# Optimization experiments

Measured on AMD Instinct MI355X. Metric: run time of the kernel, lower is better.

The kernel has to match this reference:

```python
import jax, jax.numpy as jnp
import numpy as np

N = 8192
IN_F = 128
OUT_F = 64
NEG_SLOPE = 0.2


def setup_inputs() -> dict:
    key = jax.random.key(0)
    k1, k2, k3, k4 = jax.random.split(key, 4)
    x = jax.random.normal(k1, (N, IN_F), dtype=jnp.float32)
    adj = jax.random.randint(k2, (N, N), 0, 2, dtype=jnp.int32)
    W = jax.random.normal(k3, (IN_F, OUT_F), dtype=jnp.float32) * (1.414 / np.sqrt(IN_F))
    a = jax.random.normal(k4, (2 * OUT_F, 1), dtype=jnp.float32) * 0.5
    return {"x": x, "adj": adj, "W": W, "a": a}


def reference(x, adj, W, a):
    # Wh: [N, F]
    Wh = x @ W
    # Decomposed pairwise score: e_ij = leaky_relu(Wh_i . a1 + Wh_j . a2)
    # identical math to the original [N*N, 2F] concat @ a construction.
    a1 = a[:OUT_F, 0]   # [F]
    a2 = a[OUT_F:, 0]   # [F]
    s1 = Wh @ a1        # [N]
    s2 = Wh @ a2        # [N]
    e = jax.nn.leaky_relu(s1[:, None] + s2[None, :], negative_slope=NEG_SLOPE)  # [N, N]
    # NOTE: the original zeros out non-edges (NOT -inf) before softmax.
    att = jnp.where(adj > 0, e, jnp.zeros_like(e))
    att = jax.nn.softmax(att, axis=1)
    return att @ Wh  # [N, F]
```

## Files before the change

kernel.cpp:

```cpp
#include <hip/hip_runtime.h>
#include <hip/hip_bf16.h>

#define N_NODES 8192
#define IN_FEAT 128
#define OUT_FEAT 64
#define NEG_SLOPE 0.2f
#define TILES (N_NODES / 16)
#define SUBC 256
#define NSUB (N_NODES / SUBC)
#define KPW 2
#define ROWPAD 272
#define BUFSZ (16 * ROWPAD)
#define LOG2E 1.44269504088896340736f

using f32x4  = __attribute__((ext_vector_type(4))) float;
using i32x4  = __attribute__((ext_vector_type(4))) int;
using bf16x8 = __attribute__((ext_vector_type(8))) short;

static __device__ __forceinline__ short f2bf(float f) {
    unsigned int u = __float_as_uint(f);
    unsigned int r = (u + 0x7FFFu + ((u >> 16) & 1u)) >> 16;
    return (short)r;
}

static __device__ __forceinline__ short f2bf_fast(float f) {
    __hip_bfloat16 h = __float2bfloat16(f);
    return __builtin_bit_cast(short, h);
}

static __device__ __forceinline__ float exp2_fast(float x) {
    return __builtin_amdgcn_exp2f(x);
}

__global__ __launch_bounds__(256) void k_wh(
    const float* __restrict__ x, const float* __restrict__ W,
    const float* __restrict__ a,
    float* __restrict__ s1, float* __restrict__ s2,
    unsigned short* __restrict__ whb)
{
    __shared__ float xs[4][IN_FEAT];
    const int wv   = threadIdx.x >> 6;
    const int lane = threadIdx.x & 63;
    const int row  = blockIdx.x * 4 + wv;

    const float2 xv = *(const float2*)(x + (size_t)row * IN_FEAT + lane * 2);
    xs[wv][lane * 2]     = xv.x;
    xs[wv][lane * 2 + 1] = xv.y;
    __syncthreads();

    float acc = 0.f;
    #pragma unroll
    for (int k = 0; k < IN_FEAT; ++k)
        acc = fmaf(xs[wv][k], W[k * OUT_FEAT + lane], acc);

    float p1 = acc * a[lane];
    float p2 = acc * a[OUT_FEAT + lane];
    #pragma unroll
    for (int off = 32; off; off >>= 1) {
        p1 += __shfl_xor(p1, off);
        p2 += __shfl_xor(p2, off);
    }
    if (lane == 0) {
        s1[row] = p1 * LOG2E;
        s2[row] = p2 * LOG2E;
    }

    const int jb = row >> 5;
    const int ri = row & 31;
    const int gl = ri >> 3;
    const int e  = ri & 7;
    const int fg = lane >> 4;
    const int cl = lane & 15;
    whb[(((size_t)(jb * 4 + fg) * 64) + (gl * 16 + cl)) * 8 + e] = (unsigned short)f2bf(acc);
}

__global__ __launch_bounds__(512, 6) void k_fused(
    const int* __restrict__ adj, const float* __restrict__ s1v,
    const float* __restrict__ s2v, const unsigned short* __restrict__ whb,
    float* __restrict__ out)
{
    __shared__ __align__(16) char lds[2 * BUFSZ + N_NODES * 4 + 256];
    char*  bufs = lds;
    float* s2l  = (float*)(lds + 2 * BUFSZ);
    float* zl   = (float*)(lds + 2 * BUFSZ + N_NODES * 4);
    float* red  = s2l;

    const int tid  = threadIdx.x;
    const int lane = tid & 63;
    const int w    = tid >> 6;
    const int tile = blockIdx.x;
    const int cl = lane & 15, g = lane >> 4;

    {
        const float* src = s2v + tid * 4;
        #pragma unroll
        for (int i = 0; i < 4; ++i)
            *(f32x4*)(s2l + tid * 4 + i * 2048) = *(const f32x4*)(src + i * 2048);
    }

    if (w < 4) {
        const int* stg = adj + ((size_t)(tile * 16 + w * 4)) * N_NODES + lane * 4;
        i32x4 ldA[4], ldB[4];

        auto issue = [&](i32x4 (&ld)[4], int c) {
            #pragma unroll
            for (int rr = 0; rr < 4; ++rr)
                ld[rr] = *(const i32x4*)(stg + (size_t)rr * N_NODES + c * SUBC);
        };
        auto pack = [&](i32x4 (&ld)[4], int c) {
            char* wbuf = bufs + (c & 1) * BUFSZ;
            #pragma unroll
            for (int rr = 0; rr < 4; ++rr) {
                i32x4 v = ld[rr];
                unsigned int d = (v[0] > 0 ? 1u : 0u) | (v[1] > 0 ? 0x100u : 0u)
                               | (v[2] > 0 ? 0x10000u : 0u) | (v[3] > 0 ? 0x1000000u : 0u);
                *(unsigned int*)(wbuf + (w * 4 + rr) * ROWPAD + lane * 4) = d;
            }
        };

        issue(ldA, 0);
        issue(ldB, 1);
        pack(ldA, 0);
        asm volatile("s_waitcnt lgkmcnt(0)" ::: "memory");
        __builtin_amdgcn_s_barrier();

        for (int c = 0; c < NSUB; c += 2) {
            if (c + 2 < NSUB) issue(ldA, c + 2);
            __builtin_amdgcn_sched_barrier(0);
            pack(ldB, c + 1);
            __builtin_amdgcn_sched_barrier(0);
            asm volatile("s_waitcnt lgkmcnt(0)" ::: "memory");
            __builtin_amdgcn_s_barrier();
            if (c + 3 < NSUB) issue(ldB, c + 3);
            __builtin_amdgcn_sched_barrier(0);
            if (c + 2 < NSUB) pack(ldA, c + 2);
            __builtin_amdgcn_sched_barrier(0);
            asm volatile("s_waitcnt lgkmcnt(0)" ::: "memory");
            __builtin_amdgcn_s_barrier();
        }

        __builtin_amdgcn_s_barrier();
        f32x4 rs = {0.f, 0.f, 0.f, 0.f};
        #pragma unroll
        for (int w2 = 0; w2 < 4; ++w2)
            rs += *(const f32x4*)(red + ((size_t)(w2 * 64 + lane)) * 16 + 4 * w);
        #pragma unroll
        for (int q = 0; q < 4; ++q) {
            const int rit = g * 4 + q;
            const float z = zl[rit] + zl[16 + rit] + zl[32 + rit] + zl[48 + rit];
            out[(size_t)(tile * 16 + rit) * OUT_FEAT + w * 16 + cl] = rs[q] / z;
        }
    } else {
        const int cw  = w - 4;
        const int row = tile * 16 + cl;
        const float s1r = s1v[row];

        f32x4 acc0 = {0.f, 0.f, 0.f, 0.f};
        f32x4 acc1 = acc0, acc2 = acc0, acc3 = acc0;
        float zacc = 0.f;

        asm volatile("s_waitcnt lgkmcnt(0)" ::: "memory");
        __builtin_amdgcn_s_barrier();

        for (int c = 0; c < NSUB; ++c) {
            const char* rbuf = bufs + (c & 1) * BUFSZ;
            #pragma unroll
            for (int kk = 0; kk < KPW; ++kk) {
                const int ks = cw * KPW + kk;
                const uint2 ab = *(const uint2*)(rbuf + cl * ROWPAD + ks * 32 + 8 * g);
                const float* sp = s2l + c * SUBC + ks * 32 + 8 * g;
                const f32x4 s0  = *(const f32x4*)(sp);
                const f32x4 s1x = *(const f32x4*)(sp + 4);
                const unsigned short* wq = whb + ((size_t)(c * 8 + ks)) * 2048 + lane * 8;
                bf16x8 B0 = *(const bf16x8*)(wq);
                bf16x8 B1 = *(const bf16x8*)(wq + 512);
                bf16x8 B2 = *(const bf16x8*)(wq + 1024);
                bf16x8 B3 = *(const bf16x8*)(wq + 1536);

                bf16x8 af;
                #pragma unroll
                for (int e = 0; e < 4; ++e) {
                    float tv = s1r + s0[e];
                    float el = fmaxf(tv, NEG_SLOPE * tv);
                    float wv = ((ab.x >> (8 * e)) & 1u) ? exp2_fast(el) : 1.0f;
                    zacc += wv;
                    af[e] = f2bf_fast(wv);
                }
                #pragma unroll
                for (int e = 0; e < 4; ++e) {
                    float tv = s1r + s1x[e];
                    float el = fmaxf(tv, NEG_SLOPE * tv);
                    float wv = ((ab.y >> (8 * e)) & 1u) ? exp2_fast(el) : 1.0f;
                    zacc += wv;
                    af[4 + e] = f2bf_fast(wv);
                }

                acc0 = __builtin_amdgcn_mfma_f32_16x16x32_bf16(af, B0, acc0, 0, 0, 0);
                acc1 = __builtin_amdgcn_mfma_f32_16x16x32_bf16(af, B1, acc1, 0, 0, 0);
                acc2 = __builtin_amdgcn_mfma_f32_16x16x32_bf16(af, B2, acc2, 0, 0, 0);
                acc3 = __builtin_amdgcn_mfma_f32_16x16x32_bf16(af, B3, acc3, 0, 0, 0);
            }
            asm volatile("s_waitcnt lgkmcnt(0)" ::: "memory");
            __builtin_amdgcn_s_barrier();
        }

        *(f32x4*)(red + ((size_t)(cw * 64 + lane)) * 16 + 0)  = acc0;
        *(f32x4*)(red + ((size_t)(cw * 64 + lane)) * 16 + 4)  = acc1;
        *(f32x4*)(red + ((size_t)(cw * 64 + lane)) * 16 + 8)  = acc2;
        *(f32x4*)(red + ((size_t)(cw * 64 + lane)) * 16 + 12) = acc3;
        float zz = zacc + __shfl_xor(zacc, 16);
        zz += __shfl_xor(zz, 32);
        if (lane < 16) zl[cw * 16 + lane] = zz;
        asm volatile("s_waitcnt lgkmcnt(0)" ::: "memory");
        __builtin_amdgcn_s_barrier();
    }
}

extern "C" void kernel_launch(void* const* d_in, const int* in_sizes, int n_in,
                              void* d_out, int out_size, void* d_ws, size_t ws_size,
                              hipStream_t stream) {
    const float* x   = (const float*)d_in[0];
    const int*   adj = (const int*)d_in[1];
    const float* W   = (const float*)d_in[2];
    const float* a   = (const float*)d_in[3];
    float* out = (float*)d_out;

    char* ws = (char*)d_ws;
    float* s1 = (float*)(ws);
    float* s2 = (float*)(ws + 32 * 1024);
    unsigned short* whb = (unsigned short*)(ws + 64 * 1024);

    k_wh   <<<dim3(N_NODES / 4), dim3(256), 0, stream>>>(x, W, a, s1, s2, whb);
    k_fused<<<dim3(TILES), dim3(512), 0, stream>>>(adj, s1, s2, whb, out);
}
```

Baseline: 74.34 us.

## Deepen adjacency prefetch ring to four buffers with eight producer waves

Raises the block size to 768 threads so that eight producer waves, instead of four, each load two adjacency rows. Each wave now keeps four sub-chunks of global loads in flight instead of two, and the LDS bitmask buffer ring grows from two to four slots. The aim is to hide more HBM latency on the dominant adjacency stream (256 MB of int32). The cost is more threads and more LDS per block, which may reduce how many blocks fit on a CU, plus extra idle waves during the epilogue.

After: 75.95 us. 2.2% more time.

```diff
diff --git a/kernel.cpp b/kernel.cpp
--- a/kernel.cpp
+++ b/kernel.cpp
@@ -9,6 +9,7 @@
 #define SUBC 256
 #define NSUB (N_NODES / SUBC)
 #define KPW 2
+#define RING 4
 #define ROWPAD 272
 #define BUFSZ (16 * ROWPAD)
 #define LOG2E 1.44269504088896340736f
@@ -74,15 +75,15 @@
     whb[(((size_t)(jb * 4 + fg) * 64) + (gl * 16 + cl)) * 8 + e] = (unsigned short)f2bf(acc);
 }
 
-__global__ __launch_bounds__(512, 6) void k_fused(
+__global__ __launch_bounds__(768, 6) void k_fused(
     const int* __restrict__ adj, const float* __restrict__ s1v,
     const float* __restrict__ s2v, const unsigned short* __restrict__ whb,
     float* __restrict__ out)
 {
-    __shared__ __align__(16) char lds[2 * BUFSZ + N_NODES * 4 + 256];
+    __shared__ __align__(16) char lds[RING * BUFSZ + N_NODES * 4 + 256];
     char*  bufs = lds;
-    float* s2l  = (float*)(lds + 2 * BUFSZ);
-    float* zl   = (float*)(lds + 2 * BUFSZ + N_NODES * 4);
+    float* s2l  = (float*)(lds + RING * BUFSZ);
+    float* zl   = (float*)(lds + RING * BUFSZ + N_NODES * 4);
     float* red  = s2l;
 
     const int tid  = threadIdx.x;
@@ -91,67 +92,70 @@
     const int tile = blockIdx.x;
     const int cl = lane & 15, g = lane >> 4;
 
-    {
+    if (tid < 512) {
         const float* src = s2v + tid * 4;
         #pragma unroll
         for (int i = 0; i < 4; ++i)
             *(f32x4*)(s2l + tid * 4 + i * 2048) = *(const f32x4*)(src + i * 2048);
     }
 
-    if (w < 4) {
-        const int* stg = adj + ((size_t)(tile * 16 + w * 4)) * N_NODES + lane * 4;
-        i32x4 ldA[4], ldB[4];
-
-        auto issue = [&](i32x4 (&ld)[4], int c) {
-            #pragma unroll
-            for (int rr = 0; rr < 4; ++rr)
-                ld[rr] = *(const i32x4*)(stg + (size_t)rr * N_NODES + c * SUBC);
+    if (w < 8) {
+        const int* stg = adj + ((size_t)(tile * 16 + w * 2)) * N_NODES + lane * 4;
+        i32x4 ldA[2], ldB[2], ldC[2], ldD[2];
+
+        auto issue = [&](i32x4 (&ld)[2], int c) {
+            ld[0] = *(const i32x4*)(stg + c * SUBC);
+            ld[1] = *(const i32x4*)(stg + (size_t)N_NODES + c * SUBC);
         };
-        auto pack = [&](i32x4 (&ld)[4], int c) {
-            char* wbuf = bufs + (c & 1) * BUFSZ;
-            #pragma unroll
-            for (int rr = 0; rr < 4; ++rr) {
+        auto pack = [&](i32x4 (&ld)[2], int c) {
+            char* wbuf = bufs + (c & (RING - 1)) * BUFSZ;
+            #pragma unroll
+            for (int rr = 0; rr < 2; ++rr) {
                 i32x4 v = ld[rr];
                 unsigned int d = (v[0] > 0 ? 1u : 0u) | (v[1] > 0 ? 0x100u : 0u)
                                | (v[2] > 0 ? 0x10000u : 0u) | (v[3] > 0 ? 0x1000000u : 0u);
-                *(unsigned int*)(wbuf + (w * 4 + rr) * ROWPAD + lane * 4) = d;
+                *(unsigned int*)(wbuf + (w * 2 + rr) * ROWPAD + lane * 4) = d;
             }
         };
-
-        issue(ldA, 0);
-        issue(ldB, 1);
-        pack(ldA, 0);
-        asm volatile("s_waitcnt lgkmcnt(0)" ::: "memory");
-        __builtin_amdgcn_s_barrier();
-
-        for (int c = 0; c < NSUB; c += 2) {
-            if (c + 2 < NSUB) issue(ldA, c + 2);
+        auto round_p = [&](i32x4 (&iset)[2], i32x4 (&pset)[2], int c) {
+            if (c + RING < NSUB) issue(iset, c + RING);
             __builtin_amdgcn_sched_barrier(0);
-            pack(ldB, c + 1);
+            if (c + 1 < NSUB) pack(pset, c + 1);
             __builtin_amdgcn_sched_barrier(0);
             asm volatile("s_waitcnt lgkmcnt(0)" ::: "memory");
             __builtin_amdgcn_s_barrier();
-            if (c + 3 < NSUB) issue(ldB, c + 3);
-            __builtin_amdgcn_sched_barrier(0);
-            if (c + 2 < NSUB) pack(ldA, c + 2);
-            __builtin_amdgcn_sched_barrier(0);
-            asm volatile("s_waitcnt lgkmcnt(0)" ::: "memory");
-            __builtin_amdgcn_s_barrier();
+        };
+
+        issue(ldA, 0);
+        issue(ldB, 1);
+        issue(ldC, 2);
+        issue(ldD, 3);
+        pack(ldA, 0);
+        asm volatile("s_waitcnt lgkmcnt(0)" ::: "memory");
+        __builtin_amdgcn_s_barrier();
+
+        for (int cb = 0; cb < NSUB; cb += 4) {
+            round_p(ldA, ldB, cb);
+            round_p(ldB, ldC, cb + 1);
+            round_p(ldC, ldD, cb + 2);
+            round_p(ldD, ldA, cb + 3);
         }
 
         __builtin_amdgcn_s_barrier();
-        f32x4 rs = {0.f, 0.f, 0.f, 0.f};
-        #pragma unroll
-        for (int w2 = 0; w2 < 4; ++w2)
-            rs += *(const f32x4*)(red + ((size_t)(w2 * 64 + lane)) * 16 + 4 * w);
-        #pragma unroll
-        for (int q = 0; q < 4; ++q) {
-            const int rit = g * 4 + q;
-            const float z = zl[rit] + zl[16 + rit] + zl[32 + rit] + zl[48 + rit];
-            out[(size_t)(tile * 16 + rit) * OUT_FEAT + w * 16 + cl] = rs[q] / z;
+        if (w < 4) {
+            f32x4 rs = {0.f, 0.f, 0.f, 0.f};
+            #pragma unroll
+            for (int w2 = 0; w2 < 4; ++w2)
+                rs += *(const f32x4*)(red + ((size_t)(w2 * 64 + lane)) * 16 + 4 * w);
+            #pragma unroll
+            for (int q = 0; q < 4; ++q) {
+                const int rit = g * 4 + q;
+                const float z = zl[rit] + zl[16 + rit] + zl[32 + rit] + zl[48 + rit];
+                out[(size_t)(tile * 16 + rit) * OUT_FEAT + w * 16 + cl] = rs[q] / z;
+            }
         }
     } else {
-        const int cw  = w - 4;
+        const int cw  = w - 8;
         const int row = tile * 16 + cl;
         const float s1r = s1v[row];
 
@@ -159,11 +163,10 @@
         f32x4 acc1 = acc0, acc2 = acc0, acc3 = acc0;
         float zacc = 0.f;
 
-        asm volatile("s_waitcnt lgkmcnt(0)" ::: "memory");
         __builtin_amdgcn_s_barrier();
 
         for (int c = 0; c < NSUB; ++c) {
-            const char* rbuf = bufs + (c & 1) * BUFSZ;
+            const char* rbuf = bufs + (c & (RING - 1)) * BUFSZ;
             #pragma unroll
             for (int kk = 0; kk < KPW; ++kk) {
                 const int ks = cw * KPW + kk;
@@ -231,5 +234,5 @@
     unsigned short* whb = (unsigned short*)(ws + 64 * 1024);
 
     k_wh   <<<dim3(N_NODES / 4), dim3(256), 0, stream>>>(x, W, a, s1, s2, whb);
-    k_fused<<<dim3(TILES), dim3(512), 0, stream>>>(adj, s1, s2, whb, out);
-}
+    k_fused<<<dim3(TILES), dim3(768), 0, stream>>>(adj, s1, s2, whb, out);
+}
```
